# Optimization experiments

Measured on AMD Instinct MI355X. Metric: run time of the kernel, lower is better.

The kernel has to match this reference:

```python
import jax, jax.numpy as jnp
import numpy as np

N_NODES = 500_000
N_FEAT = 125          # embedding dim; cat with pos(3) -> 128
HIDDEN = 128
OUT_DIM = 64
N_TYPES = 100
N_GRAPHS = 4096


def setup_inputs() -> dict:
    key = jax.random.key(0)
    ks = jax.random.split(key, 10)
    pos = jax.random.normal(ks[0], (N_NODES, 3), dtype=jnp.float32)
    z = jax.random.randint(ks[1], (N_NODES,), 0, N_TYPES)
    batch = jnp.sort(jax.random.randint(ks[2], (N_NODES,), 0, N_GRAPHS))
    emb = jax.random.normal(ks[3], (N_TYPES, N_FEAT), dtype=jnp.float32)
    s1 = 1.0 / np.sqrt(N_FEAT + 3)
    s2 = 1.0 / np.sqrt(HIDDEN)
    W1 = jax.random.normal(ks[4], (N_FEAT + 3, HIDDEN), dtype=jnp.float32) * s1
    b1 = jnp.zeros((HIDDEN,), dtype=jnp.float32)
    W2 = jax.random.normal(ks[5], (HIDDEN, HIDDEN), dtype=jnp.float32) * s2
    b2 = jnp.zeros((HIDDEN,), dtype=jnp.float32)
    W3 = jax.random.normal(ks[6], (HIDDEN, OUT_DIM), dtype=jnp.float32) * s2
    b3 = jnp.zeros((OUT_DIM,), dtype=jnp.float32)
    return {"pos": pos, "z": z, "batch": batch, "emb": emb,
            "W1": W1, "b1": b1, "W2": W2, "b2": b2, "W3": W3, "b3": b3}


def reference(pos, z, batch, emb, W1, b1, W2, b2, W3, b3):
    # embed node types and concat with 3D positions  -> [N, 128]
    x = jnp.concatenate([pos, emb[z]], axis=-1)
    # two equivariant-transformer layers (per-node transform) + relu
    x = jax.nn.relu(x @ W1 + b1)   # [N, H]
    x = jax.nn.relu(x @ W2 + b2)   # [N, H]
    # output head
    x = x @ W3 + b3                # [N, O]
    # global mean pool per graph
    s = jax.ops.segment_sum(x, batch, num_segments=N_GRAPHS)                    # [G, O]
    cnt = jax.ops.segment_sum(jnp.ones((x.shape[0], 1), x.dtype), batch,
                              num_segments=N_GRAPHS)                            # [G, 1]
    return s / jnp.maximum(cnt, 1.0)
```

## Files before the change

kernel.cpp:

```cpp
#include <hip/hip_runtime.h>
#include <hip/hip_bf16.h>

#define N_NODES 500000
#define N_FEAT 125
#define HID 128
#define OUTD 64
#define N_GRAPHS 4096
#define N_TYPES 100
#define NPAIRS 7813
#define NBLOCKS 256
#define NWAVES 8
#define WPAD 136

typedef float f32x4 __attribute__((ext_vector_type(4)));
typedef short s16x8 __attribute__((ext_vector_type(8)));
typedef short s16x4 __attribute__((ext_vector_type(4)));

#define OFF_T 0
#define SZ_T (N_TYPES * WPAD * 2)
#define OFF_W2 (OFF_T + SZ_T)
#define OFF_W3K (OFF_W2 + HID * WPAD * 2)
#define OFF_B2 (OFF_W3K + 4 * 8 * 64 * 8)
#define OFF_W1 (OFF_B2 + HID * 4)
#define LDS_BYTES (OFF_W1 + 3 * HID * 4)

#define WS_GSUM 0
#define WS_GCNT ((size_t)N_GRAPHS * OUTD * 4)
#define WS_T    (WS_GCNT + (size_t)N_GRAPHS * 4)
#define WS_ZERO WS_T
#define WS_ZERO_V4 (WS_ZERO / 16)

__device__ __forceinline__ unsigned short f2bf(float f) {
  union { float f; unsigned u; } v; v.f = f;
  unsigned r = v.u + 0x7FFFu + ((v.u >> 16) & 1u);
  return (unsigned short)(r >> 16);
}
__device__ __forceinline__ float bf2f(unsigned short u) {
  union { unsigned u; float f; } v; v.u = ((unsigned)u) << 16;
  return v.f;
}
__device__ __forceinline__ unsigned pk2bf(float a, float b) {
  __hip_bfloat162 h = __float22bfloat162_rn(float2{a, b});
  union { __hip_bfloat162 h; unsigned u; } v; v.h = h;
  return v.u;
}
__device__ __forceinline__ s16x4 u2frag(uint2 v) {
  union { uint2 u; s16x4 s; } c; c.u = v; return c.s;
}

extern "C" __global__ void gnn_prep(const float* __restrict__ emb,
                                    const float* __restrict__ W1,
                                    const float* __restrict__ b1,
                                    unsigned short* __restrict__ Tg,
                                    f32x4* __restrict__ wsz)
{
  const int j = threadIdx.x;
  const int tid = blockIdx.x * 128 + j;
  for (int i = tid; i < WS_ZERO_V4; i += 256 * 128)
    wsz[i] = (f32x4){0.f, 0.f, 0.f, 0.f};
  const int g = blockIdx.x;
  if (g < N_TYPES) {
    float acc = b1[j];
    const float* er = emb + g * N_FEAT;
    for (int k = 0; k < N_FEAT; ++k)
      acc = fmaf(er[k], W1[(3 + k) * HID + j], acc);
    Tg[g * HID + j] = f2bf(acc);
  }
}

extern "C" __global__ void __launch_bounds__(512, 2)
gnn_main(const float* __restrict__ pos, const int* __restrict__ z,
         const int* __restrict__ batch, const unsigned short* __restrict__ Tg,
         const float* __restrict__ W1, const float* __restrict__ W2,
         const float* __restrict__ b2, const float* __restrict__ W3,
         float* __restrict__ gsum, int* __restrict__ gcnt)
{
  extern __shared__ char lds[];
  unsigned short* Tl  = (unsigned short*)(lds + OFF_T);
  unsigned short* w2t = (unsigned short*)(lds + OFF_W2);
  uint2* w3k = (uint2*)(lds + OFF_W3K);
  float* bias2 = (float*)(lds + OFF_B2);
  float* w1l   = (float*)(lds + OFF_W1);

  const int t = threadIdx.x;

  for (int i = t; i < N_TYPES * HID; i += 512) {
    int g = i >> 7, f = i & 127;
    Tl[g * WPAD + f] = Tg[i];
  }
  for (int i = t; i < HID * HID; i += 512) {
    int k = i >> 7, n = i & 127;
    w2t[n * WPAD + k] = f2bf(W2[i]);
  }
  for (int i = t; i < 4 * 8 * 64; i += 512) {
    int ob = i >> 9, rest = i & 511;
    int oi = rest >> 6, ln = rest & 63;
    int q = ln >> 4, l = ln & 15;
    int f0 = oi * 16 + q * 4, o = ob * 16 + l;
    uint2 v;
    v.x = pk2bf(W3[(f0 + 0) * OUTD + o], W3[(f0 + 1) * OUTD + o]);
    v.y = pk2bf(W3[(f0 + 2) * OUTD + o], W3[(f0 + 3) * OUTD + o]);
    w3k[i] = v;
  }
  if (t < HID) bias2[t] = b2[t];
  if (t < 3 * HID) w1l[t] = W1[t];

  const int wave = t >> 6, lane = t & 63, quad = lane >> 4, l15 = lane & 15;

  __syncthreads();

  const int gwave = blockIdx.x * NWAVES + wave;

  for (int pair = gwave; pair < NPAIRS; pair += NBLOCKS * NWAVES) {
    const int base = pair * 64;
    const bool has2 = (pair != NPAIRS - 1);

    int id0 = batch[base + l15];
    int id1 = batch[base + 16 + l15];
    int id2 = -1, id3 = -1;
    if (has2) {
      id2 = batch[base + 32 + l15];
      id3 = batch[base + 48 + l15];
    }

    s16x8 a[4][4];
    {
      float px[4], py[4], pz[4];
      const unsigned short* Tr[4];
      #pragma unroll
      for (int m = 0; m < 4; ++m) {
        int node = base + m * 16 + l15;
        node = node < N_NODES ? node : N_NODES - 1;
        const int zi = z[node];
        px[m] = pos[node * 3]; py[m] = pos[node * 3 + 1]; pz[m] = pos[node * 3 + 2];
        Tr[m] = Tl + zi * WPAD;
      }
      #pragma unroll
      for (int k = 0; k < 4; ++k) {
        float w1s[3][8];
        #pragma unroll
        for (int c = 0; c < 3; ++c) {
          *(f32x4*)&w1s[c][0] = *(const f32x4*)(w1l + c * HID + k * 32 + quad * 8);
          *(f32x4*)&w1s[c][4] = *(const f32x4*)(w1l + c * HID + k * 32 + quad * 8 + 4);
        }
        #pragma unroll
        for (int m = 0; m < 4; ++m) {
          s16x8 tf = *(const s16x8*)(Tr[m] + k * 32 + quad * 8);
          s16x8 fr;
          #pragma unroll
          for (int j = 0; j < 8; j += 2) {
            float v0 = bf2f((unsigned short)tf[j])
                     + px[m] * w1s[0][j] + py[m] * w1s[1][j] + pz[m] * w1s[2][j];
            float v1 = bf2f((unsigned short)tf[j + 1])
                     + px[m] * w1s[0][j + 1] + py[m] * w1s[1][j + 1] + pz[m] * w1s[2][j + 1];
            ((unsigned*)&fr)[j >> 1] = pk2bf(fmaxf(v0, 0.f), fmaxf(v1, 0.f));
          }
          a[m][k] = fr;
        }
      }
    }

    uint2 pb[8][4];
    __builtin_amdgcn_s_setprio(1);
    #pragma unroll
    for (int oi = 0; oi < 8; ++oi) {
      f32x4 c[4] = {};
      #pragma unroll
      for (int k = 0; k < 4; ++k) {
        s16x8 w = *(const s16x8*)(w2t + (oi * 16 + l15) * WPAD + k * 32 + quad * 8);
        #pragma unroll
        for (int m = 0; m < 4; ++m)
          c[m] = __builtin_amdgcn_mfma_f32_16x16x32_bf16(w, a[m][k], c[m], 0, 0, 0);
      }
      const int f0 = oi * 16 + quad * 4;
      f32x4 bv = *(const f32x4*)(bias2 + f0);
      #pragma unroll
      for (int m = 0; m < 4; ++m) {
        pb[oi][m].x = pk2bf(fmaxf(c[m][0] + bv[0], 0.f), fmaxf(c[m][1] + bv[1], 0.f));
        pb[oi][m].y = pk2bf(fmaxf(c[m][2] + bv[2], 0.f), fmaxf(c[m][3] + bv[3], 0.f));
      }
    }
    __builtin_amdgcn_s_setprio(0);

    f32x4 acc3[4][4] = {};
    __builtin_amdgcn_s_setprio(1);
    #pragma unroll
    for (int ob = 0; ob < 4; ++ob)
      #pragma unroll
      for (int oi = 0; oi < 8; ++oi) {
        s16x4 wa = u2frag(w3k[(ob * 8 + oi) * 64 + lane]);
        #pragma unroll
        for (int m = 0; m < 4; ++m)
          acc3[ob][m] = __builtin_amdgcn_mfma_f32_16x16x16bf16_1k(
              wa, u2frag(pb[oi][m]), acc3[ob][m], 0, 0, 0);
      }
    __builtin_amdgcn_s_setprio(0);

    {
      const int NT = has2 ? 64 : 32;
      int done = 0;
      while (done < NT) {
        const int sel = done >> 4;
        int srcv = (sel & 2) ? ((sel & 1) ? id3 : id2)
                             : ((sel & 1) ? id1 : id0);
        const int g = __builtin_amdgcn_readlane(srcv, done & 15);
        const bool m0 = (id0 == g), m1 = (id1 == g), m2 = (id2 == g), m3 = (id3 == g);
        float red[4][4];
        #pragma unroll
        for (int ob = 0; ob < 4; ++ob)
          #pragma unroll
          for (int r = 0; r < 4; ++r)
            red[ob][r] = (m0 ? acc3[ob][0][r] : 0.f) + (m1 ? acc3[ob][1][r] : 0.f)
                       + (m2 ? acc3[ob][2][r] : 0.f) + (m3 ? acc3[ob][3][r] : 0.f);
        #pragma unroll
        for (int s = 1; s <= 8; s <<= 1)
          #pragma unroll
          for (int ob = 0; ob < 4; ++ob)
            #pragma unroll
            for (int r = 0; r < 4; ++r)
              red[ob][r] += __shfl_xor(red[ob][r], s, 64);
        const int cnt = (int)((__popcll(__ballot(m0)) + __popcll(__ballot(m1)) +
                               __popcll(__ballot(m2)) + __popcll(__ballot(m3))) >> 2);
        if (l15 == 0) {
          #pragma unroll
          for (int ob = 0; ob < 4; ++ob)
            #pragma unroll
            for (int r = 0; r < 4; ++r)
              atomicAdd(&gsum[g * OUTD + ob * 16 + quad * 4 + r], red[ob][r]);
        }
        if (lane == 0) atomicAdd(&gcnt[g], cnt);
        done += cnt;
      }
    }
  }
}

extern "C" __global__ void gnn_finalize(const float* __restrict__ gsum,
                                        const int* __restrict__ gcnt,
                                        const float* __restrict__ b3,
                                        float* __restrict__ out)
{
  int i = blockIdx.x * 256 + threadIdx.x;
  if (i < N_GRAPHS * OUTD) {
    int g = i >> 6, o = i & 63;
    int c = gcnt[g];
    out[i] = (c > 0) ? (gsum[i] / (float)c + b3[o]) : 0.f;
  }
}

extern "C" void kernel_launch(void* const* d_in, const int* in_sizes, int n_in,
                              void* d_out, int out_size, void* d_ws, size_t ws_size,
                              hipStream_t stream) {
  const float* pos  = (const float*)d_in[0];
  const int*   z    = (const int*)d_in[1];
  const int*   batch= (const int*)d_in[2];
  const float* emb  = (const float*)d_in[3];
  const float* W1   = (const float*)d_in[4];
  const float* b1   = (const float*)d_in[5];
  const float* W2   = (const float*)d_in[6];
  const float* b2   = (const float*)d_in[7];
  const float* W3   = (const float*)d_in[8];
  const float* b3   = (const float*)d_in[9];

  float* gsum = (float*)d_ws;
  int*   gcnt = (int*)((char*)d_ws + WS_GCNT);
  unsigned short* Tg = (unsigned short*)((char*)d_ws + WS_T);

  hipLaunchKernelGGL(gnn_prep, dim3(256), dim3(HID), 0, stream,
                     emb, W1, b1, Tg, (f32x4*)d_ws);

  hipFuncSetAttribute((const void*)gnn_main,
                      hipFuncAttributeMaxDynamicSharedMemorySize, LDS_BYTES);
  hipLaunchKernelGGL(gnn_main, dim3(NBLOCKS), dim3(512), LDS_BYTES, stream,
                     pos, z, batch, Tg, W1, W2, b2, W3, gsum, gcnt);
  hipLaunchKernelGGL(gnn_finalize, dim3((N_GRAPHS * OUTD + 255) / 256), dim3(256), 0, stream,
                     gsum, gcnt, b3, (float*)d_out);
}
```

Before: 132.9 us.

## Compute layer-1 position term with MFMA and chain layers in C-layout fragments

Replaces the scalar VALU computation of the first layer (type-table lookup plus a 3-wide position FMA) with a small 16x16x16 bf16 MFMA. The W1 position rows act as a zero-padded K fragment, and the fp32 type table, now kept in LDS, seeds the accumulator. Layer 2 switches to the 16x16x16 MFMA with W2 pre-swizzled into fragment layout, so layer-1 outputs feed it directly without a transpose, and the bias is folded into the accumulator init. The cost is twice as many layer-2 MFMAs at half the K, a larger fp32 table in LDS, and positions rounded to bf16.

```diff
diff --git a/kernel.cpp b/kernel.cpp
--- a/kernel.cpp
+++ b/kernel.cpp
@@ -10,19 +10,19 @@
 #define NPAIRS 7813
 #define NBLOCKS 256
 #define NWAVES 8
-#define WPAD 136
+#define TPAD 132
 
 typedef float f32x4 __attribute__((ext_vector_type(4)));
-typedef short s16x8 __attribute__((ext_vector_type(8)));
 typedef short s16x4 __attribute__((ext_vector_type(4)));
 
 #define OFF_T 0
-#define SZ_T (N_TYPES * WPAD * 2)
-#define OFF_W2 (OFF_T + SZ_T)
-#define OFF_W3K (OFF_W2 + HID * WPAD * 2)
-#define OFF_B2 (OFF_W3K + 4 * 8 * 64 * 8)
-#define OFF_W1 (OFF_B2 + HID * 4)
-#define LDS_BYTES (OFF_W1 + 3 * HID * 4)
+#define SZ_T (N_TYPES * TPAD * 4)
+#define OFF_W2K (OFF_T + SZ_T)
+#define SZ_W2K (8 * 8 * 64 * 8)
+#define OFF_W3K (OFF_W2K + SZ_W2K)
+#define SZ_W3K (4 * 8 * 64 * 8)
+#define OFF_B2 (OFF_W3K + SZ_W3K)
+#define LDS_BYTES (OFF_B2 + HID * 4)
 
 #define WS_GSUM 0
 #define WS_GCNT ((size_t)N_GRAPHS * OUTD * 4)
@@ -35,10 +35,6 @@
   unsigned r = v.u + 0x7FFFu + ((v.u >> 16) & 1u);
   return (unsigned short)(r >> 16);
 }
-__device__ __forceinline__ float bf2f(unsigned short u) {
-  union { unsigned u; float f; } v; v.u = ((unsigned)u) << 16;
-  return v.f;
-}
 __device__ __forceinline__ unsigned pk2bf(float a, float b) {
   __hip_bfloat162 h = __float22bfloat162_rn(float2{a, b});
   union { __hip_bfloat162 h; unsigned u; } v; v.h = h;
@@ -51,7 +47,7 @@
 extern "C" __global__ void gnn_prep(const float* __restrict__ emb,
                                     const float* __restrict__ W1,
                                     const float* __restrict__ b1,
-                                    unsigned short* __restrict__ Tg,
+                                    float* __restrict__ Tgf,
                                     f32x4* __restrict__ wsz)
 {
   const int j = threadIdx.x;
@@ -64,33 +60,37 @@
     const float* er = emb + g * N_FEAT;
     for (int k = 0; k < N_FEAT; ++k)
       acc = fmaf(er[k], W1[(3 + k) * HID + j], acc);
-    Tg[g * HID + j] = f2bf(acc);
+    Tgf[g * HID + j] = acc;
   }
 }
 
 extern "C" __global__ void __launch_bounds__(512, 2)
 gnn_main(const float* __restrict__ pos, const int* __restrict__ z,
-         const int* __restrict__ batch, const unsigned short* __restrict__ Tg,
+         const int* __restrict__ batch, const float* __restrict__ Tgf,
          const float* __restrict__ W1, const float* __restrict__ W2,
          const float* __restrict__ b2, const float* __restrict__ W3,
          float* __restrict__ gsum, int* __restrict__ gcnt)
 {
   extern __shared__ char lds[];
-  unsigned short* Tl  = (unsigned short*)(lds + OFF_T);
-  unsigned short* w2t = (unsigned short*)(lds + OFF_W2);
+  float* Tl = (float*)(lds + OFF_T);
+  uint2* w2k = (uint2*)(lds + OFF_W2K);
   uint2* w3k = (uint2*)(lds + OFF_W3K);
   float* bias2 = (float*)(lds + OFF_B2);
-  float* w1l   = (float*)(lds + OFF_W1);
 
   const int t = threadIdx.x;
 
   for (int i = t; i < N_TYPES * HID; i += 512) {
     int g = i >> 7, f = i & 127;
-    Tl[g * WPAD + f] = Tg[i];
-  }
-  for (int i = t; i < HID * HID; i += 512) {
-    int k = i >> 7, n = i & 127;
-    w2t[n * WPAD + k] = f2bf(W2[i]);
+    Tl[g * TPAD + f] = Tgf[i];
+  }
+  for (int i = t; i < 8 * 8 * 64; i += 512) {
+    int oi = i >> 9, ki = (i >> 6) & 7, ln = i & 63;
+    int q = ln >> 4, l = ln & 15;
+    int f0 = ki * 16 + q * 4, o = oi * 16 + l;
+    uint2 v;
+    v.x = pk2bf(W2[(f0 + 0) * HID + o], W2[(f0 + 1) * HID + o]);
+    v.y = pk2bf(W2[(f0 + 2) * HID + o], W2[(f0 + 3) * HID + o]);
+    w2k[i] = v;
   }
   for (int i = t; i < 4 * 8 * 64; i += 512) {
     int ob = i >> 9, rest = i & 511;
@@ -103,9 +103,21 @@
     w3k[i] = v;
   }
   if (t < HID) bias2[t] = b2[t];
-  if (t < 3 * HID) w1l[t] = W1[t];
 
   const int wave = t >> 6, lane = t & 63, quad = lane >> 4, l15 = lane & 15;
+
+  uint2 wa1[8];
+  #pragma unroll
+  for (int oi = 0; oi < 8; ++oi) {
+    if (quad == 0) {
+      const int f = oi * 16 + l15;
+      unsigned lo = (unsigned)f2bf(W1[f]) | ((unsigned)f2bf(W1[HID + f]) << 16);
+      unsigned hi = (unsigned)f2bf(W1[2 * HID + f]);
+      wa1[oi] = uint2{lo, hi};
+    } else {
+      wa1[oi] = uint2{0u, 0u};
+    }
+  }
 
   __syncthreads();
 
@@ -123,61 +135,49 @@
       id3 = batch[base + 48 + l15];
     }
 
-    s16x8 a[4][4];
-    {
-      float px[4], py[4], pz[4];
-      const unsigned short* Tr[4];
+    int Toff[4];
+    uint2 bpos[4];
+    #pragma unroll
+    for (int m = 0; m < 4; ++m) {
+      int node = base + m * 16 + l15;
+      node = node < N_NODES ? node : N_NODES - 1;
+      Toff[m] = z[node] * TPAD + quad * 4;
+      const float px = pos[node * 3], py = pos[node * 3 + 1], pz = pos[node * 3 + 2];
+      bpos[m] = (quad == 0) ? uint2{pk2bf(px, py), pk2bf(pz, 0.f)} : uint2{0u, 0u};
+    }
+
+    uint2 a16[8][4];
+    __builtin_amdgcn_s_setprio(1);
+    #pragma unroll
+    for (int oi = 0; oi < 8; ++oi)
       #pragma unroll
       for (int m = 0; m < 4; ++m) {
-        int node = base + m * 16 + l15;
-        node = node < N_NODES ? node : N_NODES - 1;
-        const int zi = z[node];
-        px[m] = pos[node * 3]; py[m] = pos[node * 3 + 1]; pz[m] = pos[node * 3 + 2];
-        Tr[m] = Tl + zi * WPAD;
-      }
-      #pragma unroll
-      for (int k = 0; k < 4; ++k) {
-        float w1s[3][8];
-        #pragma unroll
-        for (int c = 0; c < 3; ++c) {
-          *(f32x4*)&w1s[c][0] = *(const f32x4*)(w1l + c * HID + k * 32 + quad * 8);
-          *(f32x4*)&w1s[c][4] = *(const f32x4*)(w1l + c * HID + k * 32 + quad * 8 + 4);
-        }
-        #pragma unroll
-        for (int m = 0; m < 4; ++m) {
-          s16x8 tf = *(const s16x8*)(Tr[m] + k * 32 + quad * 8);
-          s16x8 fr;
-          #pragma unroll
-          for (int j = 0; j < 8; j += 2) {
-            float v0 = bf2f((unsigned short)tf[j])
-                     + px[m] * w1s[0][j] + py[m] * w1s[1][j] + pz[m] * w1s[2][j];
-            float v1 = bf2f((unsigned short)tf[j + 1])
-                     + px[m] * w1s[0][j + 1] + py[m] * w1s[1][j + 1] + pz[m] * w1s[2][j + 1];
-            ((unsigned*)&fr)[j >> 1] = pk2bf(fmaxf(v0, 0.f), fmaxf(v1, 0.f));
-          }
-          a[m][k] = fr;
-        }
-      }
-    }
+        f32x4 cc = *(const f32x4*)(Tl + Toff[m] + oi * 16);
+        cc = __builtin_amdgcn_mfma_f32_16x16x16bf16_1k(
+            u2frag(wa1[oi]), u2frag(bpos[m]), cc, 0, 0, 0);
+        a16[oi][m].x = pk2bf(fmaxf(cc[0], 0.f), fmaxf(cc[1], 0.f));
+        a16[oi][m].y = pk2bf(fmaxf(cc[2], 0.f), fmaxf(cc[3], 0.f));
+      }
+    __builtin_amdgcn_s_setprio(0);
 
     uint2 pb[8][4];
     __builtin_amdgcn_s_setprio(1);
     #pragma unroll
     for (int oi = 0; oi < 8; ++oi) {
-      f32x4 c[4] = {};
-      #pragma unroll
-      for (int k = 0; k < 4; ++k) {
-        s16x8 w = *(const s16x8*)(w2t + (oi * 16 + l15) * WPAD + k * 32 + quad * 8);
+      f32x4 bv = *(const f32x4*)(bias2 + oi * 16 + quad * 4);
+      f32x4 c[4] = {bv, bv, bv, bv};
+      #pragma unroll
+      for (int ki = 0; ki < 8; ++ki) {
+        s16x4 wa = u2frag(w2k[(oi * 8 + ki) * 64 + lane]);
         #pragma unroll
         for (int m = 0; m < 4; ++m)
-          c[m] = __builtin_amdgcn_mfma_f32_16x16x32_bf16(w, a[m][k], c[m], 0, 0, 0);
-      }
-      const int f0 = oi * 16 + quad * 4;
-      f32x4 bv = *(const f32x4*)(bias2 + f0);
+          c[m] = __builtin_amdgcn_mfma_f32_16x16x16bf16_1k(
+              wa, u2frag(a16[ki][m]), c[m], 0, 0, 0);
+      }
       #pragma unroll
       for (int m = 0; m < 4; ++m) {
-        pb[oi][m].x = pk2bf(fmaxf(c[m][0] + bv[0], 0.f), fmaxf(c[m][1] + bv[1], 0.f));
-        pb[oi][m].y = pk2bf(fmaxf(c[m][2] + bv[2], 0.f), fmaxf(c[m][3] + bv[3], 0.f));
+        pb[oi][m].x = pk2bf(fmaxf(c[m][0], 0.f), fmaxf(c[m][1], 0.f));
+        pb[oi][m].y = pk2bf(fmaxf(c[m][2], 0.f), fmaxf(c[m][3], 0.f));
       }
     }
     __builtin_amdgcn_s_setprio(0);
@@ -264,15 +264,15 @@
 
   float* gsum = (float*)d_ws;
   int*   gcnt = (int*)((char*)d_ws + WS_GCNT);
-  unsigned short* Tg = (unsigned short*)((char*)d_ws + WS_T);
+  float* Tgf  = (float*)((char*)d_ws + WS_T);
 
   hipLaunchKernelGGL(gnn_prep, dim3(256), dim3(HID), 0, stream,
-                     emb, W1, b1, Tg, (f32x4*)d_ws);
+                     emb, W1, b1, Tgf, (f32x4*)d_ws);
 
   hipFuncSetAttribute((const void*)gnn_main,
                       hipFuncAttributeMaxDynamicSharedMemorySize, LDS_BYTES);
   hipLaunchKernelGGL(gnn_main, dim3(NBLOCKS), dim3(512), LDS_BYTES, stream,
-                     pos, z, batch, Tg, W1, W2, b2, W3, gsum, gcnt);
+                     pos, z, batch, Tgf, W1, W2, b2, W3, gsum, gcnt);
   hipLaunchKernelGGL(gnn_finalize, dim3((N_GRAPHS * OUTD + 255) / 256), dim3(256), 0, stream,
                      gsum, gcnt, b3, (float*)d_out);
 }
```

Measured after the change: 138.1 us. 3.9% more time.

## Fuse prep, main and finalize kernels into one cooperative kernel with grid syncs

Applied to the files above, without the earlier changes.

Merges the three launches (type-table prep plus workspace zeroing, main MLP and pooling, finalize) into a single cooperative kernel. Two grid-wide barriers separate the phases, and the LDS weight staging overlaps with the prep work. This removes two kernel launch gaps. In exchange it pays for the grid sync cost and needs all 256 blocks to be co-resident.

```diff
diff --git a/kernel.cpp b/kernel.cpp
--- a/kernel.cpp
+++ b/kernel.cpp
@@ -1,5 +1,8 @@
 #include <hip/hip_runtime.h>
 #include <hip/hip_bf16.h>
+#include <hip/hip_cooperative_groups.h>
+
+namespace cg = cooperative_groups;
 
 #define N_NODES 500000
 #define N_FEAT 125
@@ -48,32 +51,14 @@
   union { uint2 u; s16x4 s; } c; c.u = v; return c.s;
 }
 
-extern "C" __global__ void gnn_prep(const float* __restrict__ emb,
-                                    const float* __restrict__ W1,
-                                    const float* __restrict__ b1,
-                                    unsigned short* __restrict__ Tg,
-                                    f32x4* __restrict__ wsz)
-{
-  const int j = threadIdx.x;
-  const int tid = blockIdx.x * 128 + j;
-  for (int i = tid; i < WS_ZERO_V4; i += 256 * 128)
-    wsz[i] = (f32x4){0.f, 0.f, 0.f, 0.f};
-  const int g = blockIdx.x;
-  if (g < N_TYPES) {
-    float acc = b1[j];
-    const float* er = emb + g * N_FEAT;
-    for (int k = 0; k < N_FEAT; ++k)
-      acc = fmaf(er[k], W1[(3 + k) * HID + j], acc);
-    Tg[g * HID + j] = f2bf(acc);
-  }
-}
-
 extern "C" __global__ void __launch_bounds__(512, 2)
-gnn_main(const float* __restrict__ pos, const int* __restrict__ z,
-         const int* __restrict__ batch, const unsigned short* __restrict__ Tg,
-         const float* __restrict__ W1, const float* __restrict__ W2,
-         const float* __restrict__ b2, const float* __restrict__ W3,
-         float* __restrict__ gsum, int* __restrict__ gcnt)
+gnn_all(const float* __restrict__ pos, const int* __restrict__ z,
+        const int* __restrict__ batch, const float* __restrict__ emb,
+        const float* __restrict__ W1, const float* __restrict__ b1,
+        const float* __restrict__ W2, const float* __restrict__ b2,
+        const float* __restrict__ W3, const float* __restrict__ b3,
+        float* __restrict__ gsum, int* __restrict__ gcnt,
+        unsigned short* __restrict__ Tg, float* __restrict__ out)
 {
   extern __shared__ char lds[];
   unsigned short* Tl  = (unsigned short*)(lds + OFF_T);
@@ -82,12 +67,21 @@
   float* bias2 = (float*)(lds + OFF_B2);
   float* w1l   = (float*)(lds + OFF_W1);
 
-  const int t = threadIdx.x;
-
-  for (int i = t; i < N_TYPES * HID; i += 512) {
-    int g = i >> 7, f = i & 127;
-    Tl[g * WPAD + f] = Tg[i];
-  }
+  const int t = threadIdx.x, bid = blockIdx.x;
+
+  {
+    f32x4* wsz = (f32x4*)gsum;
+    for (int i = bid * 512 + t; i < WS_ZERO_V4; i += NBLOCKS * 512)
+      wsz[i] = (f32x4){0.f, 0.f, 0.f, 0.f};
+    if (bid < N_TYPES && t < HID) {
+      float acc = b1[t];
+      const float* er = emb + bid * N_FEAT;
+      for (int k = 0; k < N_FEAT; ++k)
+        acc = fmaf(er[k], W1[(3 + k) * HID + t], acc);
+      Tg[bid * HID + t] = f2bf(acc);
+    }
+  }
+
   for (int i = t; i < HID * HID; i += 512) {
     int k = i >> 7, n = i & 127;
     w2t[n * WPAD + k] = f2bf(W2[i]);
@@ -105,11 +99,18 @@
   if (t < HID) bias2[t] = b2[t];
   if (t < 3 * HID) w1l[t] = W1[t];
 
+  cg::this_grid().sync();
+
+  for (int i = t; i < N_TYPES * HID; i += 512) {
+    int g = i >> 7, f = i & 127;
+    Tl[g * WPAD + f] = Tg[i];
+  }
+
   const int wave = t >> 6, lane = t & 63, quad = lane >> 4, l15 = lane & 15;
 
   __syncthreads();
 
-  const int gwave = blockIdx.x * NWAVES + wave;
+  const int gwave = bid * NWAVES + wave;
 
   for (int pair = gwave; pair < NPAIRS; pair += NBLOCKS * NWAVES) {
     const int base = pair * 64;
@@ -233,15 +234,10 @@
       }
     }
   }
-}
-
-extern "C" __global__ void gnn_finalize(const float* __restrict__ gsum,
-                                        const int* __restrict__ gcnt,
-                                        const float* __restrict__ b3,
-                                        float* __restrict__ out)
-{
-  int i = blockIdx.x * 256 + threadIdx.x;
-  if (i < N_GRAPHS * OUTD) {
+
+  cg::this_grid().sync();
+
+  for (int i = bid * 512 + t; i < N_GRAPHS * OUTD; i += NBLOCKS * 512) {
     int g = i >> 6, o = i & 63;
     int c = gcnt[g];
     out[i] = (c > 0) ? (gsum[i] / (float)c + b3[o]) : 0.f;
@@ -265,14 +261,15 @@
   float* gsum = (float*)d_ws;
   int*   gcnt = (int*)((char*)d_ws + WS_GCNT);
   unsigned short* Tg = (unsigned short*)((char*)d_ws + WS_T);
-
-  hipLaunchKernelGGL(gnn_prep, dim3(256), dim3(HID), 0, stream,
-                     emb, W1, b1, Tg, (f32x4*)d_ws);
-
-  hipFuncSetAttribute((const void*)gnn_main,
+  float* outp = (float*)d_out;
+
+  hipFuncSetAttribute((const void*)gnn_all,
                       hipFuncAttributeMaxDynamicSharedMemorySize, LDS_BYTES);
-  hipLaunchKernelGGL(gnn_main, dim3(NBLOCKS), dim3(512), LDS_BYTES, stream,
-                     pos, z, batch, Tg, W1, W2, b2, W3, gsum, gcnt);
-  hipLaunchKernelGGL(gnn_finalize, dim3((N_GRAPHS * OUTD + 255) / 256), dim3(256), 0, stream,
-                     gsum, gcnt, b3, (float*)d_out);
-}
+
+  void* args[] = {(void*)&pos, (void*)&z, (void*)&batch, (void*)&emb,
+                  (void*)&W1, (void*)&b1, (void*)&W2, (void*)&b2,
+                  (void*)&W3, (void*)&b3,
+                  (void*)&gsum, (void*)&gcnt, (void*)&Tg, (void*)&outp};
+  hipLaunchCooperativeKernel((const void*)gnn_all, dim3(NBLOCKS), dim3(512),
+                             args, LDS_BYTES, stream);
+}
```

Result: slower. 196.5 us (+47.8%).
